# Kernel tuning notes

Hardware: AMD Instinct MI355X
Metric: run time of the kernel (lower is better)

The kernel has to match this reference:

```python
import jax, jax.numpy as jnp
import numpy as np

B, S, D, H, HD = 1, 4096, 1024, 16, 64
HALF = HD // 2


def setup_inputs() -> dict:
    key = jax.random.key(0)
    ks = jax.random.split(key, 8)
    std = 0.02
    x = jax.random.normal(ks[0], (B, S, D), dtype=jnp.float32)
    wq_w = jax.random.normal(ks[1], (D, D), dtype=jnp.float32) * std
    wk_w = jax.random.normal(ks[2], (D, D), dtype=jnp.float32) * std
    wv_w = jax.random.normal(ks[3], (D, D), dtype=jnp.float32) * std
    wo_w = jax.random.normal(ks[4], (D, D), dtype=jnp.float32) * std
    wq_b = jnp.zeros((D,), jnp.float32)
    wk_b = jnp.zeros((D,), jnp.float32)
    wv_b = jnp.zeros((D,), jnp.float32)
    wo_b = jnp.zeros((D,), jnp.float32)
    # LLaMA-style rotary frequencies: theta = 10000^{-2i/HD}
    inv_freq = 1.0 / (10000.0 ** (jnp.arange(0, HD, 2, dtype=jnp.float32) / HD))  # [HALF]
    t = jnp.arange(S, dtype=jnp.float32)
    angles = jnp.outer(t, inv_freq)  # [S, HALF]
    freqs_cos = jnp.cos(angles)
    freqs_sin = jnp.sin(angles)
    # causal additive mask (finite large-negative to stay grad-safe)
    mask = jnp.triu(jnp.full((S, S), -1e9, dtype=jnp.float32), k=1)[None, None]
    return {
        "x": x, "start_pos": 0, "freqs_cos": freqs_cos, "freqs_sin": freqs_sin,
        "mask": mask,
        "wq_w": wq_w, "wq_b": wq_b, "wk_w": wk_w, "wk_b": wk_b,
        "wv_w": wv_w, "wv_b": wv_b, "wo_w": wo_w, "wo_b": wo_b,
    }


def _apply_rope(t, cos, sin):
    # t: [B, S, H, HD]; cos/sin: [S, HALF]. Complex multiply on consecutive pairs.
    b, s, h, hd = t.shape
    t2 = t.reshape(b, s, h, hd // 2, 2)
    x0, x1 = t2[..., 0], t2[..., 1]
    c = cos[None, :, None, :]
    sn = sin[None, :, None, :]
    o0 = x0 * c - x1 * sn
    o1 = x0 * sn + x1 * c
    return jnp.stack([o0, o1], axis=-1).reshape(b, s, h, hd)


def reference(x, start_pos, freqs_cos, freqs_sin, mask,
              wq_w, wq_b, wk_w, wk_b, wv_w, wv_b, wo_w, wo_b):
    bsz, seqlen, dim = x.shape
    q = (x @ wq_w.T + wq_b).reshape(bsz, seqlen, H, HD)
    k = (x @ wk_w.T + wk_b).reshape(bsz, seqlen, H, HD)
    v = (x @ wv_w.T + wv_b).reshape(bsz, seqlen, H, HD)
    q = _apply_rope(q, freqs_cos, freqs_sin)
    k = _apply_rope(k, freqs_cos, freqs_sin)
    # [B, H, S, HD]
    q = q.transpose(0, 2, 1, 3)
    k = k.transpose(0, 2, 1, 3)
    v = v.transpose(0, 2, 1, 3)
    scores = jnp.einsum('bhqd,bhkd->bhqk', q, k) / jnp.sqrt(jnp.float32(HD))
    scores = scores + mask
    probs = jax.nn.softmax(scores.astype(jnp.float32), axis=-1).astype(q.dtype)
    out = jnp.einsum('bhqk,bhkd->bhqd', probs, v)  # [B, H, S, HD]
    out = out.transpose(0, 2, 1, 3).reshape(bsz, seqlen, dim)
    return out @ wo_w.T + wo_b
```

## Files before the change

### kernel.cpp

```cpp
#include <hip/hip_runtime.h>


#define S_LEN 4096
#define DIM   1024
#define NH    16
#define HD    64

typedef __attribute__((ext_vector_type(8))) short bf16x8;
typedef __attribute__((ext_vector_type(4))) float f32x4;

__device__ __forceinline__ unsigned short f2b(float f) {
  union { float f; unsigned int u; } v; v.f = f;
  unsigned int r = (v.u + 0x7fffu + ((v.u >> 16) & 1u)) >> 16;
  return (unsigned short)r;
}
__device__ __forceinline__ float b2f(unsigned short h) {
  union { unsigned int u; float f; } v; v.u = ((unsigned int)h) << 16;
  return v.f;
}
__device__ __forceinline__ unsigned int pk2t(float a, float b) {
  union { float f; unsigned int u; } x, y; x.f = a; y.f = b;
  return (x.u >> 16) | (y.u & 0xffff0000u);
}
__device__ __forceinline__ void gload16(const void* g, void* l) {
  __builtin_amdgcn_global_load_lds(
      (const __attribute__((address_space(1))) unsigned int*)g,
      (__attribute__((address_space(3))) unsigned int*)l, 16, 0, 0);
}
__device__ __forceinline__ f32x4 fzero4() { f32x4 z = {0.f, 0.f, 0.f, 0.f}; return z; }

__device__ __forceinline__ bf16x8 lds_swz(const unsigned short* s, int row, int chunk) {
  int byte = row * 128 + ((chunk ^ (row & 7)) << 4);
  return *(const bf16x8*)((const char*)s + byte);
}

__global__ void cvt_all(const float* __restrict__ x, const float* __restrict__ wq,
                        const float* __restrict__ wk, const float* __restrict__ wv,
                        const float* __restrict__ wo, const float* __restrict__ qb,
                        const float* __restrict__ kb, const float* __restrict__ vbs,
                        const float* __restrict__ ob, unsigned short* __restrict__ xb,
                        unsigned short* __restrict__ wqkvb, unsigned short* __restrict__ wobb,
                        float* __restrict__ biasq, float* __restrict__ biaso) {
  int i = blockIdx.x * 256 + threadIdx.x;
  if (i < 2097152) {
    const float* src; unsigned short* dst; int off;
    if (i < 1048576)      { src = x;  dst = xb;              off = i; }
    else if (i < 1310720) { src = wq; dst = wqkvb;           off = i - 1048576; }
    else if (i < 1572864) { src = wk; dst = wqkvb + 1048576; off = i - 1310720; }
    else if (i < 1835008) { src = wv; dst = wqkvb + 2097152; off = i - 1572864; }
    else                  { src = wo; dst = wobb;            off = i - 1835008; }
    float4 v = ((const float4*)src)[off];
    unsigned int lo = (unsigned int)f2b(v.x) | ((unsigned int)f2b(v.y) << 16);
    unsigned int hi = (unsigned int)f2b(v.z) | ((unsigned int)f2b(v.w) << 16);
    ((uint2*)dst)[off] = make_uint2(lo, hi);
  } else if (i < 2097152 + 1024) {
    int j = i - 2097152;
    if (j < 256)      ((float4*)biasq)[j]              = ((const float4*)qb)[j];
    else if (j < 512) ((float4*)(biasq + 1024))[j-256] = ((const float4*)kb)[j-256];
    else if (j < 768) ((float4*)(biasq + 2048))[j-512] = ((const float4*)vbs)[j-512];
    else              ((float4*)biaso)[j-768]          = ((const float4*)ob)[j-768];
  }
}

__global__ __launch_bounds__(512, 2) void gemm_qkv(
    const unsigned short* __restrict__ A, const unsigned short* __restrict__ B,
    const float* __restrict__ bias, unsigned short* __restrict__ dq,
    unsigned short* __restrict__ dk, unsigned short* __restrict__ vtout,
    const float* __restrict__ fc, const float* __restrict__ fs, int K) {
  __shared__ alignas(16) unsigned short sA[2][256 * 64];
  __shared__ alignas(16) unsigned short sB[2][256 * 64];
  const int tid = threadIdx.x;
  const int lane = tid & 63, wave = tid >> 6;
  const int ln = lane & 15, quad = lane >> 4;
  const int bm = blockIdx.x * 256, bn = blockIdx.y * 256;
  const int wr = (wave >> 2) * 128, wc = (wave & 3) * 64;
  const int NT = K >> 6;

  f32x4 acc[8][4];
#pragma unroll
  for (int i = 0; i < 8; ++i)
#pragma unroll
    for (int j = 0; j < 4; ++j) acc[i][j] = fzero4();

#define STAGE(tt, ch) do {                                                   \
    int o_ = ((ch) * 512 + tid) * 8;                                         \
    int row_ = o_ >> 6, c_ = (o_ >> 3) & 7;                                  \
    int col_ = ((tt) << 6) + ((c_ ^ (row_ & 7)) << 3);                       \
    int bs_ = (tt) & 1;                                                      \
    gload16(A + (size_t)(bm + row_) * K + col_, (char*)sA[bs_] + o_ * 2);    \
    gload16(B + (size_t)(bn + row_) * K + col_, (char*)sB[bs_] + o_ * 2);    \
  } while (0)
#define BAR()   __builtin_amdgcn_s_barrier()
#define LGKM0() asm volatile("s_waitcnt lgkmcnt(0)" ::: "memory")

  STAGE(0, 0); STAGE(0, 1); STAGE(0, 2); STAGE(0, 3); STAGE(1, 0);
  asm volatile("s_waitcnt vmcnt(2)" ::: "memory");
  BAR();

#pragma unroll 2
  for (int t = 0; t < 16; ++t) {
    const unsigned short* cA = sA[t & 1];
    const unsigned short* cB = sB[t & 1];
    bf16x8 a0[4], a1[4], b0[4], b1[4];

#pragma unroll
    for (int j = 0; j < 4; ++j) b0[j] = lds_swz(cB, wc + j * 16 + ln, quad);
#pragma unroll
    for (int i = 0; i < 4; ++i) a0[i] = lds_swz(cA, wr + i * 16 + ln, quad);
    if (t + 1 < NT) STAGE(t + 1, 1);
    BAR(); LGKM0();
    __builtin_amdgcn_s_setprio(1);
#pragma unroll
    for (int i = 0; i < 4; ++i)
#pragma unroll
      for (int j = 0; j < 4; ++j)
        acc[i][j] = __builtin_amdgcn_mfma_f32_16x16x32_bf16(a0[i], b0[j], acc[i][j], 0, 0, 0);
    __builtin_amdgcn_s_setprio(0);
    BAR();

#pragma unroll
    for (int i = 0; i < 4; ++i) a1[i] = lds_swz(cA, wr + (i + 4) * 16 + ln, quad);
#pragma unroll
    for (int j = 0; j < 4; ++j) b1[j] = lds_swz(cB, wc + j * 16 + ln, 4 + quad);
    if (t + 1 < NT) STAGE(t + 1, 2);
    BAR(); LGKM0();
    __builtin_amdgcn_s_setprio(1);
#pragma unroll
    for (int i = 0; i < 4; ++i)
#pragma unroll
      for (int j = 0; j < 4; ++j)
        acc[i + 4][j] = __builtin_amdgcn_mfma_f32_16x16x32_bf16(a1[i], b0[j], acc[i + 4][j], 0, 0, 0);
    __builtin_amdgcn_s_setprio(0);
    BAR();

#pragma unroll
    for (int i = 0; i < 4; ++i) a0[i] = lds_swz(cA, wr + i * 16 + ln, 4 + quad);
#pragma unroll
    for (int i = 0; i < 4; ++i) a1[i] = lds_swz(cA, wr + (i + 4) * 16 + ln, 4 + quad);
    if (t + 1 < NT) STAGE(t + 1, 3);
    BAR(); LGKM0();
    __builtin_amdgcn_s_setprio(1);
#pragma unroll
    for (int i = 0; i < 4; ++i)
#pragma unroll
      for (int j = 0; j < 4; ++j)
        acc[i][j] = __builtin_amdgcn_mfma_f32_16x16x32_bf16(a0[i], b1[j], acc[i][j], 0, 0, 0);
    __builtin_amdgcn_s_setprio(0);
    BAR();

    if (t + 2 < NT) STAGE(t + 2, 0);
    BAR(); LGKM0();
    __builtin_amdgcn_s_setprio(1);
#pragma unroll
    for (int i = 0; i < 4; ++i)
#pragma unroll
      for (int j = 0; j < 4; ++j)
        acc[i + 4][j] = __builtin_amdgcn_mfma_f32_16x16x32_bf16(a1[i], b1[j], acc[i + 4][j], 0, 0, 0);
    __builtin_amdgcn_s_setprio(0);
    if (t < 14) {
      asm volatile("s_waitcnt vmcnt(2)" ::: "memory");
      BAR();
    } else if (t == 14) {
      asm volatile("s_waitcnt vmcnt(0)" ::: "memory");
      BAR();
    }
  }
#undef STAGE
#undef BAR
#undef LGKM0

  const int bufi = bn >> 10;
  const int hq = ((bn & 1023) + wc) >> 6;
  if (bufi < 2) {
    unsigned short* const base = bufi == 0 ? dq : dk;
    const float qsc = bufi == 0 ? 0.180336880f : 1.0f;
#pragma unroll
    for (int i = 0; i < 8; ++i)
#pragma unroll
      for (int j = 0; j < 4; ++j) {
        int n = bn + wc + j * 16 + ln;
        float bi = bias[n];
        int hd = j * 16 + ln;
        int pi = hd >> 1;
        bool evn = (ln & 1) == 0;
#pragma unroll
        for (int r = 0; r < 4; ++r) {
          int m = bm + wr + i * 16 + quad * 4 + r;
          float val = acc[i][j][r] + bi;
          float par = __shfl_xor(val, 1);
          float c = fc[m * 32 + pi], sn = fs[m * 32 + pi];
          float o = evn ? (val * c - par * sn) : (par * sn + val * c);
          base[((size_t)(hq * S_LEN + m)) * HD + hd] = f2b(o * qsc);
        }
      }
  } else {
    __syncthreads();
    unsigned short* scr =
        (wave < 4 ? (unsigned short*)sA : (unsigned short*)sB) + (wave & 3) * 8192;
#pragma unroll
    for (int i = 0; i < 8; ++i)
#pragma unroll
      for (int j = 0; j < 4; ++j) {
        int n = bn + wc + j * 16 + ln;
        float bi = bias[n];
        int hd = j * 16 + ln;
#pragma unroll
        for (int r = 0; r < 4; ++r) {
          int sl = i * 16 + quad * 4 + r;
          int byte = hd * 256 + ((((sl >> 3) ^ (hd & 7)) << 4)) + (sl & 7) * 2;
          *(unsigned short*)((char*)scr + byte) = f2b(acc[i][j][r] + bi);
        }
      }
    __syncthreads();
#pragma unroll
    for (int pass = 0; pass < 4; ++pass) {
      int row = pass * 16 + ln;
      uint4 d[4];
#pragma unroll
      for (int j = 0; j < 4; ++j) {
        int c = quad * 4 + j;
        d[j] = *(uint4*)((char*)scr + row * 256 + ((c ^ (row & 7)) << 4));
      }
      uint4* dst = (uint4*)(vtout + ((size_t)(hq * HD + row)) * S_LEN + bm + wr + quad * 32);
#pragma unroll
      for (int j = 0; j < 4; ++j) dst[j] = d[j];
    }
  }
}

__global__ __launch_bounds__(256) void gemm_out(
    const unsigned short* __restrict__ A, const unsigned short* __restrict__ B,
    const float* __restrict__ bias, float* __restrict__ outF, int N, int K) {
  __shared__ alignas(16) unsigned short sA[2][128 * 32];
  __shared__ alignas(16) unsigned short sB[2][64 * 32];
  const int tid = threadIdx.x;
  const int lane = tid & 63, wave = tid >> 6;
  const int ln = lane & 15, quad = lane >> 4;
  const int bm = blockIdx.x * 128, bn = blockIdx.y * 64;
  const int wr = (wave >> 1) * 64, wc = (wave & 1) * 32;

  f32x4 acc[4][2];
#pragma unroll
  for (int i = 0; i < 4; ++i)
#pragma unroll
    for (int j = 0; j < 2; ++j) acc[i][j] = fzero4();

  {
#pragma unroll
    for (int i = 0; i < 2; ++i) {
      int o = (i * 256 + tid) * 16;
      int e = o >> 1;
      int row = e >> 5, col = e & 31;
      gload16(A + (size_t)(bm + row) * K + col, (char*)sA[0] + o);
    }
    int o = tid * 16;
    int e = o >> 1;
    int row = e >> 5, col = e & 31;
    gload16(B + (size_t)(bn + row) * K + col, (char*)sB[0] + o);
  }

  int buf = 0;
  for (int k0 = 0; k0 < K; k0 += 32, buf ^= 1) {
    __syncthreads();
    if (k0 + 32 < K) {
#pragma unroll
      for (int i = 0; i < 2; ++i) {
        int o = (i * 256 + tid) * 16;
        int e = o >> 1;
        int row = e >> 5, col = e & 31;
        gload16(A + (size_t)(bm + row) * K + k0 + 32 + col, (char*)sA[buf ^ 1] + o);
      }
      int o = tid * 16;
      int e = o >> 1;
      int row = e >> 5, col = e & 31;
      gload16(B + (size_t)(bn + row) * K + k0 + 32 + col, (char*)sB[buf ^ 1] + o);
    }
    bf16x8 af[4], bfr[2];
#pragma unroll
    for (int i = 0; i < 4; ++i)
      af[i] = *(const bf16x8*)&sA[buf][(wr + i * 16 + ln) * 32 + quad * 8];
#pragma unroll
    for (int j = 0; j < 2; ++j)
      bfr[j] = *(const bf16x8*)&sB[buf][(wc + j * 16 + ln) * 32 + quad * 8];
#pragma unroll
    for (int i = 0; i < 4; ++i)
#pragma unroll
      for (int j = 0; j < 2; ++j)
        acc[i][j] = __builtin_amdgcn_mfma_f32_16x16x32_bf16(af[i], bfr[j], acc[i][j], 0, 0, 0);
  }

#pragma unroll
  for (int i = 0; i < 4; ++i)
#pragma unroll
    for (int j = 0; j < 2; ++j) {
      int n = bn + wc + j * 16 + ln;
      float bi = bias[n];
#pragma unroll
      for (int r = 0; r < 4; ++r) {
        int m = bm + wr + i * 16 + quad * 4 + r;
        outF[(size_t)m * N + n] = acc[i][j][r] + bi;
      }
    }
}

__global__ __launch_bounds__(512, 4) void flash_kernel(
    const unsigned short* __restrict__ qg, const unsigned short* __restrict__ kg,
    const unsigned short* __restrict__ vtg, unsigned short* __restrict__ attn) {
  __shared__ alignas(16) unsigned short sK[2][2][64 * 64];
  __shared__ alignas(16) unsigned short sV[2][2][64 * 64];

  const int tid = threadIdx.x;
  const int lane = tid & 63, wave = tid >> 6;
  const int w = wave & 3, grp = wave >> 2;
  const int ln = lane & 15, quad = lane >> 4;
  const int c = blockIdx.x;
  const int h = c & 15;
  const int qt = 63 - (c >> 4);
  const int qrow = qt * 64 + w * 16;

  const unsigned short* qh = qg + (size_t)h * (S_LEN * HD);
  const unsigned short* kh = kg + (size_t)h * (S_LEN * HD);
  const unsigned short* vh = vtg + (size_t)h * (HD * S_LEN);

  bf16x8 qf[2];
  qf[0] = *(const bf16x8*)(qh + (size_t)(qrow + ln) * HD + quad * 8);
  qf[1] = *(const bf16x8*)(qh + (size_t)(qrow + ln) * HD + 32 + quad * 8);

  f32x4 o_acc[4];
  f32x4 l_acc = fzero4();
#pragma unroll
  for (int t = 0; t < 4; ++t) o_acc[t] = fzero4();
  bf16x8 ones;
#pragma unroll
  for (int j = 0; j < 8; ++j) ones[j] = (short)0x3F80;

  const int nst = (qt + 2) >> 1;
  const int srow = tid >> 3, sch = tid & 7;
  const int kswz = (sch ^ (srow & 7)) << 3;

  gload16(kh + (size_t)srow * HD + kswz, (char*)sK[0][0] + tid * 16);
  gload16(kh + (size_t)(64 + srow) * HD + kswz, (char*)sK[0][1] + tid * 16);
  gload16(vh + (size_t)srow * S_LEN + kswz, (char*)sV[0][0] + tid * 16);
  gload16(vh + (size_t)srow * S_LEN + 64 + kswz, (char*)sV[0][1] + tid * 16);

  int buf = 0;
  for (int s = 0; s < nst; ++s, buf ^= 1) {
    __syncthreads();
    if (s + 1 < nst) {
      const int kvE = (2 * s + 2) * 64, kvO = kvE + 64;
      gload16(kh + (size_t)(kvE + srow) * HD + kswz, (char*)sK[buf ^ 1][0] + tid * 16);
      gload16(kh + (size_t)(kvO + srow) * HD + kswz, (char*)sK[buf ^ 1][1] + tid * 16);
      gload16(vh + (size_t)srow * S_LEN + kvE + kswz, (char*)sV[buf ^ 1][0] + tid * 16);
      gload16(vh + (size_t)srow * S_LEN + kvO + kswz, (char*)sV[buf ^ 1][1] + tid * 16);
    }
    const int kt = 2 * s + grp;
    if (kt > qt) continue;
    const unsigned short* kp = sK[buf][grp];
    const unsigned short* vp = sV[buf][grp];

    f32x4 sc[4];
#pragma unroll
    for (int t = 0; t < 4; ++t) sc[t] = fzero4();
#pragma unroll
    for (int t = 0; t < 4; ++t) {
      bf16x8 kb0 = lds_swz(kp, t * 16 + ln, quad);
      bf16x8 kb1 = lds_swz(kp, t * 16 + ln, 4 + quad);
      sc[t] = __builtin_amdgcn_mfma_f32_16x16x32_bf16(kb0, qf[0], sc[t], 0, 0, 0);
      sc[t] = __builtin_amdgcn_mfma_f32_16x16x32_bf16(kb1, qf[1], sc[t], 0, 0, 0);
    }

    float e[4][4];
    if (kt == qt) {
#pragma unroll
      for (int t = 0; t < 4; ++t)
#pragma unroll
        for (int r = 0; r < 4; ++r) {
          int kvl = 16 * t + quad * 4 + r;
          e[t][r] = (kvl <= w * 16 + ln) ? __builtin_amdgcn_exp2f(sc[t][r]) : 0.0f;
        }
    } else {
#pragma unroll
      for (int t = 0; t < 4; ++t)
#pragma unroll
        for (int r = 0; r < 4; ++r) e[t][r] = __builtin_amdgcn_exp2f(sc[t][r]);
    }

    unsigned int x0 = pk2t(e[0][0], e[0][1]), x1 = pk2t(e[0][2], e[0][3]);
    unsigned int y0 = pk2t(e[1][0], e[1][1]), y1 = pk2t(e[1][2], e[1][3]);
    unsigned int z0 = pk2t(e[2][0], e[2][1]), z1 = pk2t(e[2][2], e[2][3]);
    unsigned int w0 = pk2t(e[3][0], e[3][1]), w1 = pk2t(e[3][2], e[3][3]);
    auto a32 = __builtin_amdgcn_permlane32_swap(x0, y0, false, false);
    auto a16 = __builtin_amdgcn_permlane16_swap(a32[0], a32[1], false, false);
    auto b32 = __builtin_amdgcn_permlane32_swap(x1, y1, false, false);
    auto b16 = __builtin_amdgcn_permlane16_swap(b32[0], b32[1], false, false);
    auto c32 = __builtin_amdgcn_permlane32_swap(z0, w0, false, false);
    auto c16 = __builtin_amdgcn_permlane16_swap(c32[0], c32[1], false, false);
    auto d32 = __builtin_amdgcn_permlane32_swap(z1, w1, false, false);
    auto d16 = __builtin_amdgcn_permlane16_swap(d32[0], d32[1], false, false);
    union { uint4 u; bf16x8 b; } pa0u, pa1u;
    pa0u.u = make_uint4(a16[0], b16[0], a16[1], b16[1]);
    pa1u.u = make_uint4(c16[0], d16[0], c16[1], d16[1]);
    const bf16x8 pa0 = pa0u.b, pa1 = pa1u.b;

    l_acc = __builtin_amdgcn_mfma_f32_16x16x32_bf16(pa0, ones, l_acc, 0, 0, 0);
    l_acc = __builtin_amdgcn_mfma_f32_16x16x32_bf16(pa1, ones, l_acc, 0, 0, 0);

#pragma unroll
    for (int t = 0; t < 4; ++t) {
      bf16x8 vb0 = lds_swz(vp, t * 16 + ln, quad);
      bf16x8 vb1 = lds_swz(vp, t * 16 + ln, 4 + quad);
      o_acc[t] = __builtin_amdgcn_mfma_f32_16x16x32_bf16(pa0, vb0, o_acc[t], 0, 0, 0);
      o_acc[t] = __builtin_amdgcn_mfma_f32_16x16x32_bf16(pa1, vb1, o_acc[t], 0, 0, 0);
    }
  }

  __syncthreads();
  float* mrg = (float*)sK;
  const int mi = (w * 64 + lane) * 20;
  if (grp == 1) {
    *(f32x4*)&mrg[mi +  0] = o_acc[0];
    *(f32x4*)&mrg[mi +  4] = o_acc[1];
    *(f32x4*)&mrg[mi +  8] = o_acc[2];
    *(f32x4*)&mrg[mi + 12] = o_acc[3];
    *(f32x4*)&mrg[mi + 16] = l_acc;
  }
  __syncthreads();
  if (grp == 0) {
    o_acc[0] += *(const f32x4*)&mrg[mi + 0];
    o_acc[1] += *(const f32x4*)&mrg[mi + 4];
    o_acc[2] += *(const f32x4*)&mrg[mi + 8];
    o_acc[3] += *(const f32x4*)&mrg[mi + 12];
    l_acc += *(const f32x4*)&mrg[mi + 16];
    float inv[4];
#pragma unroll
    for (int r = 0; r < 4; ++r) inv[r] = 1.0f / l_acc[r];
#pragma unroll
    for (int t = 0; t < 4; ++t)
#pragma unroll
      for (int r = 0; r < 4; ++r) {
        int row = qrow + quad * 4 + r;
        attn[(size_t)row * DIM + h * HD + t * 16 + ln] = f2b(o_acc[t][r] * inv[r]);
      }
  }
}

extern "C" void kernel_launch(void* const* d_in, const int* in_sizes, int n_in,
                              void* d_out, int out_size, void* d_ws, size_t ws_size,
                              hipStream_t stream) {
  const float* x    = (const float*)d_in[0];
  const float* fc   = (const float*)d_in[2];
  const float* fs   = (const float*)d_in[3];
  const float* wqw  = (const float*)d_in[5];
  const float* wqb  = (const float*)d_in[6];
  const float* wkw  = (const float*)d_in[7];
  const float* wkb  = (const float*)d_in[8];
  const float* wvw  = (const float*)d_in[9];
  const float* wvb  = (const float*)d_in[10];
  const float* wow  = (const float*)d_in[11];
  const float* wobf = (const float*)d_in[12];
  float* out = (float*)d_out;

  char* ws = (char*)d_ws;
  const size_t MB = (size_t)1 << 20;
  unsigned short* xb    = (unsigned short*)(ws + 0);
  unsigned short* wqkvb = (unsigned short*)(ws + 8 * MB);
  unsigned short* wobb  = (unsigned short*)(ws + 16 * MB);
  float* biasq = (float*)(ws + 18 * MB);
  float* biaso = (float*)(ws + 18 * MB + 65536);
  unsigned short* qb_ = (unsigned short*)(ws + 19 * MB);
  unsigned short* kb_ = (unsigned short*)(ws + 27 * MB);
  unsigned short* vt  = (unsigned short*)(ws + 35 * MB);
  unsigned short* attn = (unsigned short*)(ws + 0);

  cvt_all<<<8196, 256, 0, stream>>>(x, wqw, wkw, wvw, wow, wqb, wkb, wvb, wobf,
                                    xb, wqkvb, wobb, biasq, biaso);
  gemm_qkv<<<dim3(16, 12), 512, 0, stream>>>(xb, wqkvb, biasq, qb_, kb_, vt, fc, fs, 1024);
  flash_kernel<<<1024, 512, 0, stream>>>(qb_, kb_, vt, attn);
  gemm_out<<<dim3(32, 16), 256, 0, stream>>>(attn, wobb, biaso, out, 1024, 1024);
}
```

Before: 248.2 us.

## Drop KV-split wave groups in flash kernel; use 32-row KV tiles with 256 threads

Flash attention blocks go from 8 waves, where two groups split the KV tiles and merge results through shared memory, to 4 waves that each walk every KV tile in 32-row steps. Each step double-buffers a 32x64 K tile and a 64x32 V^T tile with a new swizzle, and the causal skip and mask now work per wave at 32-key granularity. This removes the cross-group merge, its two barriers and the wasted group-1 iterations on the diagonal, and allows more blocks per CU. The cost is twice as many loop iterations and barriers per block, with smaller MFMA batches per barrier.

```diff
diff --git a/kernel.cpp b/kernel.cpp
--- a/kernel.cpp
+++ b/kernel.cpp
@@ -303,20 +303,19 @@
     }
 }
 
-__global__ __launch_bounds__(512, 4) void flash_kernel(
+__global__ __launch_bounds__(256, 8) void flash_kernel(
     const unsigned short* __restrict__ qg, const unsigned short* __restrict__ kg,
     const unsigned short* __restrict__ vtg, unsigned short* __restrict__ attn) {
-  __shared__ alignas(16) unsigned short sK[2][2][64 * 64];
-  __shared__ alignas(16) unsigned short sV[2][2][64 * 64];
+  __shared__ alignas(16) unsigned short sK[2][32 * 64];
+  __shared__ alignas(16) unsigned short sV[2][64 * 32];
 
   const int tid = threadIdx.x;
   const int lane = tid & 63, wave = tid >> 6;
-  const int w = wave & 3, grp = wave >> 2;
   const int ln = lane & 15, quad = lane >> 4;
   const int c = blockIdx.x;
   const int h = c & 15;
   const int qt = 63 - (c >> 4);
-  const int qrow = qt * 64 + w * 16;
+  const int qrow = qt * 64 + wave * 16;
 
   const unsigned short* qh = qg + (size_t)h * (S_LEN * HD);
   const unsigned short* kh = kg + (size_t)h * (S_LEN * HD);
@@ -334,114 +333,85 @@
 #pragma unroll
   for (int j = 0; j < 8; ++j) ones[j] = (short)0x3F80;
 
-  const int nst = (qt + 2) >> 1;
-  const int srow = tid >> 3, sch = tid & 7;
-  const int kswz = (sch ^ (srow & 7)) << 3;
-
-  gload16(kh + (size_t)srow * HD + kswz, (char*)sK[0][0] + tid * 16);
-  gload16(kh + (size_t)(64 + srow) * HD + kswz, (char*)sK[0][1] + tid * 16);
-  gload16(vh + (size_t)srow * S_LEN + kswz, (char*)sV[0][0] + tid * 16);
-  gload16(vh + (size_t)srow * S_LEN + 64 + kswz, (char*)sV[0][1] + tid * 16);
+  const int nkv = 2 * qt + 2;
+  const int krow = tid >> 3, kch = tid & 7;
+  const int vrow = tid >> 2, vch = tid & 3;
+  const unsigned short* ksrc = kh + (size_t)krow * HD + ((kch ^ (krow & 7)) << 3);
+  const unsigned short* vsrc = vh + (size_t)vrow * S_LEN + ((vch ^ ((vrow >> 1) & 3)) << 3);
+
+  gload16(ksrc, (char*)sK[0] + tid * 16);
+  gload16(vsrc, (char*)sV[0] + tid * 16);
 
   int buf = 0;
-  for (int s = 0; s < nst; ++s, buf ^= 1) {
+  for (int s = 0; s < nkv; ++s, buf ^= 1) {
     __syncthreads();
-    if (s + 1 < nst) {
-      const int kvE = (2 * s + 2) * 64, kvO = kvE + 64;
-      gload16(kh + (size_t)(kvE + srow) * HD + kswz, (char*)sK[buf ^ 1][0] + tid * 16);
-      gload16(kh + (size_t)(kvO + srow) * HD + kswz, (char*)sK[buf ^ 1][1] + tid * 16);
-      gload16(vh + (size_t)srow * S_LEN + kvE + kswz, (char*)sV[buf ^ 1][0] + tid * 16);
-      gload16(vh + (size_t)srow * S_LEN + kvO + kswz, (char*)sV[buf ^ 1][1] + tid * 16);
-    }
-    const int kt = 2 * s + grp;
-    if (kt > qt) continue;
-    const unsigned short* kp = sK[buf][grp];
-    const unsigned short* vp = sV[buf][grp];
-
-    f32x4 sc[4];
-#pragma unroll
-    for (int t = 0; t < 4; ++t) sc[t] = fzero4();
-#pragma unroll
-    for (int t = 0; t < 4; ++t) {
+    if (s + 1 < nkv) {
+      gload16(ksrc + (size_t)(s + 1) * (32 * HD), (char*)sK[buf ^ 1] + tid * 16);
+      gload16(vsrc + (size_t)(s + 1) * 32, (char*)sV[buf ^ 1] + tid * 16);
+    }
+    const int kv0 = s * 32;
+    if (kv0 > qrow + 15) continue;
+    const unsigned short* kp = sK[buf];
+    const unsigned short* vp = sV[buf];
+
+    f32x4 sc[2];
+#pragma unroll
+    for (int t = 0; t < 2; ++t) {
+      sc[t] = fzero4();
       bf16x8 kb0 = lds_swz(kp, t * 16 + ln, quad);
       bf16x8 kb1 = lds_swz(kp, t * 16 + ln, 4 + quad);
       sc[t] = __builtin_amdgcn_mfma_f32_16x16x32_bf16(kb0, qf[0], sc[t], 0, 0, 0);
       sc[t] = __builtin_amdgcn_mfma_f32_16x16x32_bf16(kb1, qf[1], sc[t], 0, 0, 0);
     }
 
-    float e[4][4];
-    if (kt == qt) {
-#pragma unroll
-      for (int t = 0; t < 4; ++t)
+    float e[2][4];
+    if (kv0 + 31 > qrow) {
+      const int dql = (qrow - kv0) + ln;
+#pragma unroll
+      for (int t = 0; t < 2; ++t)
 #pragma unroll
         for (int r = 0; r < 4; ++r) {
           int kvl = 16 * t + quad * 4 + r;
-          e[t][r] = (kvl <= w * 16 + ln) ? __builtin_amdgcn_exp2f(sc[t][r]) : 0.0f;
+          e[t][r] = (kvl <= dql) ? __builtin_amdgcn_exp2f(sc[t][r]) : 0.0f;
         }
     } else {
 #pragma unroll
-      for (int t = 0; t < 4; ++t)
+      for (int t = 0; t < 2; ++t)
 #pragma unroll
         for (int r = 0; r < 4; ++r) e[t][r] = __builtin_amdgcn_exp2f(sc[t][r]);
     }
 
     unsigned int x0 = pk2t(e[0][0], e[0][1]), x1 = pk2t(e[0][2], e[0][3]);
     unsigned int y0 = pk2t(e[1][0], e[1][1]), y1 = pk2t(e[1][2], e[1][3]);
-    unsigned int z0 = pk2t(e[2][0], e[2][1]), z1 = pk2t(e[2][2], e[2][3]);
-    unsigned int w0 = pk2t(e[3][0], e[3][1]), w1 = pk2t(e[3][2], e[3][3]);
     auto a32 = __builtin_amdgcn_permlane32_swap(x0, y0, false, false);
     auto a16 = __builtin_amdgcn_permlane16_swap(a32[0], a32[1], false, false);
     auto b32 = __builtin_amdgcn_permlane32_swap(x1, y1, false, false);
     auto b16 = __builtin_amdgcn_permlane16_swap(b32[0], b32[1], false, false);
-    auto c32 = __builtin_amdgcn_permlane32_swap(z0, w0, false, false);
-    auto c16 = __builtin_amdgcn_permlane16_swap(c32[0], c32[1], false, false);
-    auto d32 = __builtin_amdgcn_permlane32_swap(z1, w1, false, false);
-    auto d16 = __builtin_amdgcn_permlane16_swap(d32[0], d32[1], false, false);
-    union { uint4 u; bf16x8 b; } pa0u, pa1u;
-    pa0u.u = make_uint4(a16[0], b16[0], a16[1], b16[1]);
-    pa1u.u = make_uint4(c16[0], d16[0], c16[1], d16[1]);
-    const bf16x8 pa0 = pa0u.b, pa1 = pa1u.b;
-
-    l_acc = __builtin_amdgcn_mfma_f32_16x16x32_bf16(pa0, ones, l_acc, 0, 0, 0);
-    l_acc = __builtin_amdgcn_mfma_f32_16x16x32_bf16(pa1, ones, l_acc, 0, 0, 0);
+    union { uint4 u; bf16x8 b; } pau;
+    pau.u = make_uint4(a16[0], b16[0], a16[1], b16[1]);
+    const bf16x8 pa = pau.b;
+
+    l_acc = __builtin_amdgcn_mfma_f32_16x16x32_bf16(pa, ones, l_acc, 0, 0, 0);
 
 #pragma unroll
     for (int t = 0; t < 4; ++t) {
-      bf16x8 vb0 = lds_swz(vp, t * 16 + ln, quad);
-      bf16x8 vb1 = lds_swz(vp, t * 16 + ln, 4 + quad);
-      o_acc[t] = __builtin_amdgcn_mfma_f32_16x16x32_bf16(pa0, vb0, o_acc[t], 0, 0, 0);
-      o_acc[t] = __builtin_amdgcn_mfma_f32_16x16x32_bf16(pa1, vb1, o_acc[t], 0, 0, 0);
-    }
-  }
-
-  __syncthreads();
-  float* mrg = (float*)sK;
-  const int mi = (w * 64 + lane) * 20;
-  if (grp == 1) {
-    *(f32x4*)&mrg[mi +  0] = o_acc[0];
-    *(f32x4*)&mrg[mi +  4] = o_acc[1];
-    *(f32x4*)&mrg[mi +  8] = o_acc[2];
-    *(f32x4*)&mrg[mi + 12] = o_acc[3];
-    *(f32x4*)&mrg[mi + 16] = l_acc;
-  }
-  __syncthreads();
-  if (grp == 0) {
-    o_acc[0] += *(const f32x4*)&mrg[mi + 0];
-    o_acc[1] += *(const f32x4*)&mrg[mi + 4];
-    o_acc[2] += *(const f32x4*)&mrg[mi + 8];
-    o_acc[3] += *(const f32x4*)&mrg[mi + 12];
-    l_acc += *(const f32x4*)&mrg[mi + 16];
-    float inv[4];
-#pragma unroll
-    for (int r = 0; r < 4; ++r) inv[r] = 1.0f / l_acc[r];
-#pragma unroll
-    for (int t = 0; t < 4; ++t)
-#pragma unroll
-      for (int r = 0; r < 4; ++r) {
-        int row = qrow + quad * 4 + r;
-        attn[(size_t)row * DIM + h * HD + t * 16 + ln] = f2b(o_acc[t][r] * inv[r]);
-      }
-  }
+      int vr = t * 16 + ln;
+      bf16x8 vb = *(const bf16x8*)((const char*)vp + vr * 64 +
+                                   ((quad ^ ((vr >> 1) & 3)) << 4));
+      o_acc[t] = __builtin_amdgcn_mfma_f32_16x16x32_bf16(pa, vb, o_acc[t], 0, 0, 0);
+    }
+  }
+
+  float inv[4];
+#pragma unroll
+  for (int r = 0; r < 4; ++r) inv[r] = 1.0f / l_acc[r];
+#pragma unroll
+  for (int t = 0; t < 4; ++t)
+#pragma unroll
+    for (int r = 0; r < 4; ++r) {
+      int row = qrow + quad * 4 + r;
+      attn[(size_t)row * DIM + h * HD + t * 16 + ln] = f2b(o_acc[t][r] * inv[r]);
+    }
 }
 
 extern "C" void kernel_launch(void* const* d_in, const int* in_sizes, int n_in,
@@ -475,6 +445,6 @@
   cvt_all<<<8196, 256, 0, stream>>>(x, wqw, wkw, wvw, wow, wqb, wkb, wvb, wobf,
                                     xb, wqkvb, wobb, biasq, biaso);
   gemm_qkv<<<dim3(16, 12), 512, 0, stream>>>(xb, wqkvb, biasq, qb_, kb_, vt, fc, fs, 1024);
-  flash_kernel<<<1024, 512, 0, stream>>>(qb_, kb_, vt, attn);
+  flash_kernel<<<1024, 256, 0, stream>>>(qb_, kb_, vt, attn);
   gemm_out<<<dim3(32, 16), 256, 0, stream>>>(attn, wobb, biaso, out, 1024, 1024);
 }
```

Result: slower. 284.3 us (+14.5%).

## Drop KV split-in-half across wave groups in flash kernel; use 256-thread blocks

Applied to the files above, without the earlier changes.

The flash attention kernel previously used 8 waves, with two groups each processing alternate KV tiles, then merged partial accumulators through LDS. It now uses 4 waves per block, each walking every KV tile sequentially, which removes the merge step, its two barriers, and half the shared memory per block. Block-to-query-tile mapping is also permuted so work is interleaved across heavy and light causal tiles. The trade-off is twice as many serial KV iterations per wave, with less per-block parallelism to hide latency, partly offset by the higher occupancy target of 6 blocks.

```diff
diff --git a/kernel.cpp b/kernel.cpp
--- a/kernel.cpp
+++ b/kernel.cpp
@@ -303,20 +303,20 @@
     }
 }
 
-__global__ __launch_bounds__(512, 4) void flash_kernel(
+__global__ __launch_bounds__(256, 6) void flash_kernel(
     const unsigned short* __restrict__ qg, const unsigned short* __restrict__ kg,
     const unsigned short* __restrict__ vtg, unsigned short* __restrict__ attn) {
-  __shared__ alignas(16) unsigned short sK[2][2][64 * 64];
-  __shared__ alignas(16) unsigned short sV[2][2][64 * 64];
+  __shared__ alignas(16) unsigned short sK[2][64 * 64];
+  __shared__ alignas(16) unsigned short sV[2][64 * 64];
 
   const int tid = threadIdx.x;
   const int lane = tid & 63, wave = tid >> 6;
-  const int w = wave & 3, grp = wave >> 2;
   const int ln = lane & 15, quad = lane >> 4;
   const int c = blockIdx.x;
   const int h = c & 15;
-  const int qt = 63 - (c >> 4);
-  const int qrow = qt * 64 + w * 16;
+  const int u0 = (c >> 4) & 15, jj = c >> 8;
+  const int qt = (jj == 0) ? u0 : (jj == 1) ? 31 - u0 : (jj == 2) ? 32 + u0 : 63 - u0;
+  const int qrow = qt * 64 + wave * 16;
 
   const unsigned short* qh = qg + (size_t)h * (S_LEN * HD);
   const unsigned short* kh = kg + (size_t)h * (S_LEN * HD);
@@ -334,35 +334,40 @@
 #pragma unroll
   for (int j = 0; j < 8; ++j) ones[j] = (short)0x3F80;
 
-  const int nst = (qt + 2) >> 1;
-  const int srow = tid >> 3, sch = tid & 7;
-  const int kswz = (sch ^ (srow & 7)) << 3;
-
-  gload16(kh + (size_t)srow * HD + kswz, (char*)sK[0][0] + tid * 16);
-  gload16(kh + (size_t)(64 + srow) * HD + kswz, (char*)sK[0][1] + tid * 16);
-  gload16(vh + (size_t)srow * S_LEN + kswz, (char*)sV[0][0] + tid * 16);
-  gload16(vh + (size_t)srow * S_LEN + 64 + kswz, (char*)sV[0][1] + tid * 16);
+  int kof[2], vof[2], ldst[2];
+#pragma unroll
+  for (int i = 0; i < 2; ++i) {
+    int idx = i * 256 + tid;
+    int row = idx >> 3, ch = idx & 7;
+    int sw = (ch ^ (row & 7)) << 3;
+    kof[i] = row * HD + sw;
+    vof[i] = row * S_LEN + sw;
+    ldst[i] = idx * 16;
+  }
+
+#pragma unroll
+  for (int i = 0; i < 2; ++i) {
+    gload16(kh + kof[i], (char*)sK[0] + ldst[i]);
+    gload16(vh + vof[i], (char*)sV[0] + ldst[i]);
+  }
 
   int buf = 0;
-  for (int s = 0; s < nst; ++s, buf ^= 1) {
+  for (int s = 0; s <= qt; ++s, buf ^= 1) {
     __syncthreads();
-    if (s + 1 < nst) {
-      const int kvE = (2 * s + 2) * 64, kvO = kvE + 64;
-      gload16(kh + (size_t)(kvE + srow) * HD + kswz, (char*)sK[buf ^ 1][0] + tid * 16);
-      gload16(kh + (size_t)(kvO + srow) * HD + kswz, (char*)sK[buf ^ 1][1] + tid * 16);
-      gload16(vh + (size_t)srow * S_LEN + kvE + kswz, (char*)sV[buf ^ 1][0] + tid * 16);
-      gload16(vh + (size_t)srow * S_LEN + kvO + kswz, (char*)sV[buf ^ 1][1] + tid * 16);
-    }
-    const int kt = 2 * s + grp;
-    if (kt > qt) continue;
-    const unsigned short* kp = sK[buf][grp];
-    const unsigned short* vp = sV[buf][grp];
+    if (s < qt) {
+#pragma unroll
+      for (int i = 0; i < 2; ++i) {
+        gload16(kh + (size_t)(s + 1) * (64 * HD) + kof[i], (char*)sK[buf ^ 1] + ldst[i]);
+        gload16(vh + (size_t)(s + 1) * 64 + vof[i], (char*)sV[buf ^ 1] + ldst[i]);
+      }
+    }
+    const unsigned short* kp = sK[buf];
+    const unsigned short* vp = sV[buf];
 
     f32x4 sc[4];
 #pragma unroll
-    for (int t = 0; t < 4; ++t) sc[t] = fzero4();
-#pragma unroll
     for (int t = 0; t < 4; ++t) {
+      sc[t] = fzero4();
       bf16x8 kb0 = lds_swz(kp, t * 16 + ln, quad);
       bf16x8 kb1 = lds_swz(kp, t * 16 + ln, 4 + quad);
       sc[t] = __builtin_amdgcn_mfma_f32_16x16x32_bf16(kb0, qf[0], sc[t], 0, 0, 0);
@@ -370,13 +375,14 @@
     }
 
     float e[4][4];
-    if (kt == qt) {
+    if (s == qt) {
+      const int dql = wave * 16 + ln;
 #pragma unroll
       for (int t = 0; t < 4; ++t)
 #pragma unroll
         for (int r = 0; r < 4; ++r) {
           int kvl = 16 * t + quad * 4 + r;
-          e[t][r] = (kvl <= w * 16 + ln) ? __builtin_amdgcn_exp2f(sc[t][r]) : 0.0f;
+          e[t][r] = (kvl <= dql) ? __builtin_amdgcn_exp2f(sc[t][r]) : 0.0f;
         }
     } else {
 #pragma unroll
@@ -414,34 +420,16 @@
     }
   }
 
-  __syncthreads();
-  float* mrg = (float*)sK;
-  const int mi = (w * 64 + lane) * 20;
-  if (grp == 1) {
-    *(f32x4*)&mrg[mi +  0] = o_acc[0];
-    *(f32x4*)&mrg[mi +  4] = o_acc[1];
-    *(f32x4*)&mrg[mi +  8] = o_acc[2];
-    *(f32x4*)&mrg[mi + 12] = o_acc[3];
-    *(f32x4*)&mrg[mi + 16] = l_acc;
-  }
-  __syncthreads();
-  if (grp == 0) {
-    o_acc[0] += *(const f32x4*)&mrg[mi + 0];
-    o_acc[1] += *(const f32x4*)&mrg[mi + 4];
-    o_acc[2] += *(const f32x4*)&mrg[mi + 8];
-    o_acc[3] += *(const f32x4*)&mrg[mi + 12];
-    l_acc += *(const f32x4*)&mrg[mi + 16];
-    float inv[4];
-#pragma unroll
-    for (int r = 0; r < 4; ++r) inv[r] = 1.0f / l_acc[r];
-#pragma unroll
-    for (int t = 0; t < 4; ++t)
-#pragma unroll
-      for (int r = 0; r < 4; ++r) {
-        int row = qrow + quad * 4 + r;
-        attn[(size_t)row * DIM + h * HD + t * 16 + ln] = f2b(o_acc[t][r] * inv[r]);
-      }
-  }
+  float inv[4];
+#pragma unroll
+  for (int r = 0; r < 4; ++r) inv[r] = 1.0f / l_acc[r];
+#pragma unroll
+  for (int t = 0; t < 4; ++t)
+#pragma unroll
+    for (int r = 0; r < 4; ++r) {
+      int row = qrow + quad * 4 + r;
+      attn[(size_t)row * DIM + h * HD + t * 16 + ln] = f2b(o_acc[t][r] * inv[r]);
+    }
 }
 
 extern "C" void kernel_launch(void* const* d_in, const int* in_sizes, int n_in,
@@ -475,6 +463,6 @@
   cvt_all<<<8196, 256, 0, stream>>>(x, wqw, wkw, wvw, wow, wqb, wkb, wvb, wobf,
                                     xb, wqkvb, wobb, biasq, biaso);
   gemm_qkv<<<dim3(16, 12), 512, 0, stream>>>(xb, wqkvb, biasq, qb_, kb_, vt, fc, fs, 1024);
-  flash_kernel<<<1024, 512, 0, stream>>>(qb_, kb_, vt, attn);
+  flash_kernel<<<1024, 256, 0, stream>>>(qb_, kb_, vt, attn);
   gemm_out<<<dim3(32, 16), 256, 0, stream>>>(attn, wobb, biaso, out, 1024, 1024);
 }
```

Result: slower. 268.7 us (+8.2%).
